# Optimization experiments

Hardware: AMD Instinct MI355X
Metric: run time of the kernel (lower is better)

The kernel has to match this reference:

```python
import jax, jax.numpy as jnp
import numpy as np

EPS = 1e-12  # F.normalize default eps

def _l2norm(x):
    n = jnp.linalg.norm(x, axis=-1, keepdims=True)
    return x / jnp.maximum(n, EPS)

def setup_inputs() -> dict:
    key = jax.random.key(0)
    k1, k2, k3 = jax.random.split(key, 3)
    Q, N, d_key, d_val = 4096, 65536, 128, 128
    return {
        "q": jax.random.normal(k1, (Q, d_key), dtype=jnp.float32),
        "keys": jax.random.normal(k2, (N, d_key), dtype=jnp.float32),
        "vals": jax.random.normal(k3, (N, d_val), dtype=jnp.float32),
        "topk": 8,
    }

def reference(q, keys, vals, topk):
    # cosine similarity: normalize both sides then dense matmul
    kn = _l2norm(keys)            # [N, d_key]
    qn = _l2norm(q)               # [Q, d_key]
    sims = qn @ kn.T              # [Q, N]
    kk = min(topk, sims.shape[1])
    topv, topi = jax.lax.top_k(sims, kk)          # [Q, k], [Q, k]
    weights = jax.nn.softmax(topv, axis=-1)        # [Q, k]
    gathered = vals[topi]                          # [Q, k, d_val] gather
    pred = jnp.einsum('qb,qbd->qd', weights, gathered)
    conf = jnp.clip(jnp.mean(topv, axis=-1), 0.0, 1.0)
    return pred, conf
```

## Files before the change

kernel.cpp:

```cpp
#include <hip/hip_runtime.h>
#include <stdint.h>


typedef unsigned int u32;
typedef unsigned long long u64;
typedef unsigned short u16;
typedef __attribute__((ext_vector_type(4))) float f32x4;
typedef __attribute__((ext_vector_type(2))) float f32x2;
typedef __attribute__((ext_vector_type(4))) int i32x4;
typedef __attribute__((ext_vector_type(8))) short s16x8;

#define D 128
#define KTILE 64
#define QW 64
#define QB 256
#define CMAX 64
#define MARGIN 0.05f
#define TBYTES (KTILE * 256)

__device__ __forceinline__ u16 f2bf(float f) {
    u32 b = __float_as_uint(f);
    b += 0x7FFFu + ((b >> 16) & 1u);
    return (u16)(b >> 16);
}
__device__ __forceinline__ u32 ford(float f) {
    u32 b = __float_as_uint(f);
    return (b & 0x80000000u) ? ~b : (b | 0x80000000u);
}
__device__ __forceinline__ float ford_inv(u32 ob) {
    u32 b = (ob & 0x80000000u) ? (ob ^ 0x80000000u) : ~ob;
    return __uint_as_float(b);
}

__global__ __launch_bounds__(256) void k_norm_keys(
        const float* __restrict__ keys, const float* __restrict__ q,
        u16* __restrict__ kn, float* __restrict__ invk, u16* __restrict__ qbf,
        int N, int Q) {
    int row = blockIdx.x * 4 + (threadIdx.x >> 6);
    int lane = threadIdx.x & 63;
    if (row >= N) return;
    if (row < Q) {
        f32x2 qv = *(const f32x2*)(q + (size_t)row * D + lane * 2);
        u32 qp = (u32)f2bf(qv.x) | ((u32)f2bf(qv.y) << 16);
        *(u32*)(qbf + (size_t)row * D + lane * 2) = qp;
    }
    const float* kr = keys + (size_t)row * D;
    f32x2 v = *(const f32x2*)(kr + lane * 2);
    float ss = v.x * v.x + v.y * v.y;
    #pragma unroll
    for (int o = 1; o < 64; o <<= 1) ss += __shfl_xor(ss, o);
    float inv = 1.0f / fmaxf(sqrtf(ss), 1e-12f);
    if (lane == 0) invk[row] = inv;
    u32 packed = (u32)f2bf(v.x * inv) | ((u32)f2bf(v.y * inv) << 16);
    *(u32*)(kn + (size_t)row * D + lane * 2) = packed;
}

__device__ __forceinline__ void load_afr_bf(const u16* qbf, int qrow_base,
                                            int lrow, int lhi, s16x8 afr[4]) {
    const u16* qrow = qbf + (size_t)(qrow_base + lrow) * D + lhi * 8;
    #pragma unroll
    for (int s = 0; s < 4; ++s) afr[s] = *(const s16x8*)(qrow + s * 32);
}

__device__ __forceinline__ void decode_bid(int bid, int nqb, int PPART,
                                           int& p, int& qb) {
    if ((PPART & 7) == 0) {
        int xcd = bid & 7, seq = bid >> 3;
        qb = seq % nqb;
        p  = (seq / nqb) * 8 + xcd;
    } else {
        p = bid / nqb; qb = bid % nqb;
    }
}


__global__ __launch_bounds__(256, 2) void k_pass1(
        const u16* __restrict__ kn, const u16* __restrict__ qbf,
        float* __restrict__ shi, float* __restrict__ ssec,
        int Q, int N, int PPART) {
    __shared__ __align__(16) char lds[TBYTES];
    const int tid = threadIdx.x;
    const int wave = tid >> 6, lane = tid & 63;
    const int lrow = lane & 15, lhi = lane >> 4;
    const int nqb = Q / QB;
    int p, qb;
    decode_bid(blockIdx.x, nqb, PPART, p, qb);
    const int part = N / PPART;
    const int key0 = p * part;
    const int qbase = qb * QB + wave * QW;

    s16x8 afr[4][4];
    #pragma unroll
    for (int qs = 0; qs < 4; ++qs) load_afr_bf(qbf, qbase + qs * 16, lrow, lhi, afr[qs]);

    float hi[4][4], sec[4][4];
    #pragma unroll
    for (int qs = 0; qs < 4; ++qs)
        #pragma unroll
        for (int r = 0; r < 4; ++r) { hi[qs][r] = -3.0e38f; sec[qs][r] = -3.0e38f; }

    int roff[4];
    #pragma unroll
    for (int s = 0; s < 4; ++s)
        roff[s] = lrow * 256 + ((((s << 2) + lhi) ^ lrow) << 4);

    const int srow = tid >> 2;
    const int sg0  = (tid & 3) << 2;
    const int sx   = srow & 15;
    int woff[4];
    #pragma unroll
    for (int i = 0; i < 4; ++i) woff[i] = srow * 256 + (((sg0 + i) ^ sx) << 4);
    const char* gsrc = (const char*)kn + ((size_t)(key0 + srow)) * 256 + sg0 * 16;

    const int iters = part / KTILE;
    i32x4 v[4];
    #pragma unroll
    for (int i = 0; i < 4; ++i) v[i] = *(const i32x4*)(gsrc + i * 16);
    const char* gnext = gsrc + TBYTES;

    const f32x4 kZero = {0.f, 0.f, 0.f, 0.f};

    for (int kb = 0; kb < iters; ++kb) {
        __syncthreads();
        #pragma unroll
        for (int i = 0; i < 4; ++i) *(i32x4*)(lds + woff[i]) = v[i];
        __syncthreads();
        if (kb + 1 < iters) {
            #pragma unroll
            for (int i = 0; i < 4; ++i) v[i] = *(const i32x4*)(gnext + i * 16);
            gnext += TBYTES;
        }
        __builtin_amdgcn_s_setprio(1);
        #pragma unroll
        for (int ktp = 0; ktp < 2; ++ktp) {
            const u32 tagA = (u32)((kb << 2) + (ktp << 1));
            const u32 tagB = tagA + 1u;
            s16x8 bfrA[4], bfrB[4];
            #pragma unroll
            for (int s = 0; s < 4; ++s) {
                bfrA[s] = *(const s16x8*)(lds + roff[s] + (ktp << 1) * 4096);
                bfrB[s] = *(const s16x8*)(lds + roff[s] + ((ktp << 1) + 1) * 4096);
            }
            #pragma unroll
            for (int qs = 0; qs < 4; ++qs) {
                f32x4 accA = __builtin_amdgcn_mfma_f32_16x16x32_bf16(
                                 afr[qs][0], bfrA[0], kZero, 0, 0, 0);
                f32x4 accB = __builtin_amdgcn_mfma_f32_16x16x32_bf16(
                                 afr[qs][0], bfrB[0], kZero, 0, 0, 0);
                #pragma unroll
                for (int s = 1; s < 4; ++s) {
                    accA = __builtin_amdgcn_mfma_f32_16x16x32_bf16(afr[qs][s], bfrA[s], accA, 0, 0, 0);
                    accB = __builtin_amdgcn_mfma_f32_16x16x32_bf16(afr[qs][s], bfrB[s], accB, 0, 0, 0);
                }
                #pragma unroll
                for (int r = 0; r < 4; ++r) {
                    float fa = __uint_as_float(
                        (__float_as_uint(accA[r]) & 0xFFFFFF00u) | tagA);
                    float fb = __uint_as_float(
                        (__float_as_uint(accB[r]) & 0xFFFFFF00u) | tagB);
                    float h0 = hi[qs][r];
                    sec[qs][r] = fmaxf(__builtin_amdgcn_fmed3f(h0, fa, fb), sec[qs][r]);
                    hi[qs][r]  = fmaxf(fmaxf(h0, fa), fb);
                }
            }
        }
        __builtin_amdgcn_s_setprio(0);
    }
    #pragma unroll
    for (int qs = 0; qs < 4; ++qs)
        #pragma unroll
        for (int r = 0; r < 4; ++r) {
            int qq = qbase + qs * 16 + (lhi << 2) + r;
            shi [((size_t)p * Q + qq) * 16 + lrow] = hi[qs][r];
            ssec[((size_t)p * Q + qq) * 16 + lrow] = sec[qs][r];
        }
}

__global__ __launch_bounds__(256) void k_finalize(
        const float* __restrict__ q, const float* __restrict__ keys,
        const float* __restrict__ vals, const float* __restrict__ invk,
        const float* __restrict__ shi, const float* __restrict__ ssec,
        float* __restrict__ pred, float* __restrict__ conf,
        int Q, int N, int PPART) {
    const int w = threadIdx.x >> 6;
    const int qq = blockIdx.x * 4 + w;
    const int lane = threadIdx.x & 63;
    __shared__ float qs[4][D];
    __shared__ u32 cand[4][CMAX];
    __shared__ u32 ccnt[4];
    if (lane == 0) ccnt[w] = 0u;

    const float* qrow = q + (size_t)qq * D;
    f32x2 qv = *(const f32x2*)(qrow + lane * 2);
    qs[w][lane * 2] = qv.x; qs[w][lane * 2 + 1] = qv.y;
    float ss = qv.x * qv.x + qv.y * qv.y;
    #pragma unroll
    for (int o = 1; o < 64; o <<= 1) ss += __shfl_xor(ss, o);
    const float invq = 1.0f / fmaxf(sqrtf(ss), 1e-12f);

    const int nv = PPART >> 2;
    float v[16], hv[16], sc[16];
    #pragma unroll
    for (int i = 0; i < 16; ++i) {
        if (i < nv) {
            size_t base = ((size_t)(i * 4 + (lane >> 4)) * Q + qq) * 16 + (lane & 15);
            hv[i] = v[i] = shi[base];
            sc[i] = ssec[base];
        } else { hv[i] = v[i] = sc[i] = -3.0e38f; }
    }
    float h = -3.0e38f;
    #pragma unroll
    for (int round = 0; round < 8; ++round) {
        h = v[0];
        #pragma unroll
        for (int i = 1; i < 16; ++i) h = fmaxf(h, v[i]);
        #pragma unroll
        for (int o = 1; o < 64; o <<= 1) h = fmaxf(h, __shfl_xor(h, o));
        #pragma unroll
        for (int i = 0; i < 16; ++i) if (v[i] == h) v[i] = -3.0e38f;
    }
    const float T = h - MARGIN;
    const int part = N / PPART;
    #pragma unroll
    for (int i = 0; i < 16; ++i) {
        if (i >= nv) break;
        const int sidx = i * 64 + lane;
        const int p = sidx >> 4, j = sidx & 15;
        if (hv[i] >= T) {
            u32 key = (u32)(p * part + (int)((__float_as_uint(hv[i]) & 255u) << 4) + j);
            u32 pos = atomicAdd(&ccnt[w], 1u);
            if (pos < CMAX) cand[w][pos] = key;
        }
        if (sc[i] >= T) {
            u32 key = (u32)(p * part + (int)((__float_as_uint(sc[i]) & 255u) << 4) + j);
            u32 pos = atomicAdd(&ccnt[w], 1u);
            if (pos < CMAX) cand[w][pos] = key;
        }
    }
    __syncthreads();

    const u32 n = min(ccnt[w], (u32)CMAX);
    const int c0 = lane >> 1;
    const int half = lane & 1;
    const bool valid0 = (u32)c0 < n;
    const bool valid1 = (u32)(c0 + 32) < n;
    const u32 key0 = valid0 ? cand[w][c0] : 0u;
    const u32 key1 = valid1 ? cand[w][c0 + 32] : 0u;

    const float* qsp = &qs[w][half * 64];
    float dot0 = 0.f, dot1 = 0.f;
    {
        const float* kr0 = keys + (size_t)key0 * D + half * 64;
        const float* kr1 = keys + (size_t)key1 * D + half * 64;
        #pragma unroll
        for (int j = 0; j < 64; j += 4) {
            f32x4 a = *(const f32x4*)(kr0 + j);
            f32x4 b = *(const f32x4*)(kr1 + j);
            dot0 += a.x * qsp[j] + a.y * qsp[j + 1] + a.z * qsp[j + 2] + a.w * qsp[j + 3];
            dot1 += b.x * qsp[j] + b.y * qsp[j + 1] + b.z * qsp[j + 2] + b.w * qsp[j + 3];
        }
    }
    dot0 += __shfl_xor(dot0, 1);
    dot1 += __shfl_xor(dot1, 1);
    const float ex0 = dot0 * invk[key0] * invq;
    const float ex1 = dot1 * invk[key1] * invq;
    u64 pkA = valid0 ? (((u64)ford(ex0) << 32) | (u32)(~key0)) : 0ull;
    u64 pkB = valid1 ? (((u64)ford(ex1) << 32) | (u32)(~key1)) : 0ull;

    float accA = 0.f, accB = 0.f, wsum = 0.f, vsum = 0.f, vmax = 0.f;
    #pragma unroll
    for (int r = 0; r < 8; ++r) {
        u64 mx = pkA > pkB ? pkA : pkB;
        u64 hh = mx;
        #pragma unroll
        for (int o = 1; o < 64; o <<= 1) {
            u64 tt = __shfl_xor(hh, o);
            hh = tt > hh ? tt : hh;
        }
        const bool ok = (hh != 0ull);
        const float vv = ford_inv((u32)(hh >> 32));
        const u32 idx = ok ? ~((u32)hh) : 0u;
        if (r == 0) vmax = vv;
        const float wgt = ok ? expf(vv - vmax) : 0.f;
        wsum += wgt; vsum += ok ? vv : 0.f;
        const float* vr = vals + (size_t)idx * D;
        accA += wgt * vr[lane];
        accB += wgt * vr[lane + 64];
        if (pkA == hh) pkA = 0ull;
        if (pkB == hh) pkB = 0ull;
    }
    const float inv_ws = 1.0f / wsum;
    pred[(size_t)qq * D + lane] = accA * inv_ws;
    pred[(size_t)qq * D + lane + 64] = accB * inv_ws;
    if (lane == 0) conf[qq] = fminf(fmaxf(vsum * 0.125f, 0.f), 1.f);
}

extern "C" void kernel_launch(void* const* d_in, const int* in_sizes, int n_in,
                              void* d_out, int out_size, void* d_ws, size_t ws_size,
                              hipStream_t stream) {
    const float* q    = (const float*)d_in[0];
    const float* keys = (const float*)d_in[1];
    const float* vals = (const float*)d_in[2];
    const int Q = in_sizes[0] / D;
    const int N = in_sizes[1] / D;

    int PPART = 64;
    auto need = [&](int P) {
        return (size_t)N * D * 2 + (size_t)N * 4 + (size_t)Q * D * 2 +
               2 * ((size_t)Q * P * 16 * 4);
    };
    while (PPART > 16 && need(PPART) > ws_size) PPART >>= 1;

    char* ws = (char*)d_ws;
    size_t off = 0;
    u16*   kn   = (u16*)(ws + off);   off += (size_t)N * D * 2;
    float* invk = (float*)(ws + off); off += (size_t)N * 4;
    u16*   qbf  = (u16*)(ws + off);   off += (size_t)Q * D * 2;
    float* shi  = (float*)(ws + off); off += (size_t)Q * PPART * 16 * 4;
    float* ssec = (float*)(ws + off); off += (size_t)Q * PPART * 16 * 4;

    float* pred = (float*)d_out;
    float* conf = pred + (size_t)Q * D;

    k_norm_keys<<<(N + 3) / 4, 256, 0, stream>>>(keys, q, kn, invk, qbf, N, Q);
    k_pass1<<<(Q / QB) * PPART, 256, 0, stream>>>(kn, qbf, shi, ssec, Q, N, PPART);
    k_finalize<<<Q / 4, 256, 0, stream>>>(q, keys, vals, invk, shi, ssec,
                                          pred, conf, Q, N, PPART);
}
```

Measured before the change: 106.0 us.

## Merge paired key tiles before top-2 tracking, expand candidates to both keys

The similarity pass now takes the max of the two paired MFMA results (tiles A and B) before tagging and updating the running top-2. This roughly halves the per-element tag and compare work in the hot loop. In exchange, each surviving tag now stands for two possible keys, so the finalize kernel enqueues both keys per hit. CMAX rises from 64 to 96 and a third candidate slot per lane is added for exact rescoring, which adds more gathers and dot products in finalize.

```diff
diff --git a/kernel.cpp b/kernel.cpp
--- a/kernel.cpp
+++ b/kernel.cpp
@@ -14,7 +14,7 @@
 #define KTILE 64
 #define QW 64
 #define QB 256
-#define CMAX 64
+#define CMAX 96
 #define MARGIN 0.05f
 #define TBYTES (KTILE * 256)
 
@@ -133,8 +133,7 @@
         __builtin_amdgcn_s_setprio(1);
         #pragma unroll
         for (int ktp = 0; ktp < 2; ++ktp) {
-            const u32 tagA = (u32)((kb << 2) + (ktp << 1));
-            const u32 tagB = tagA + 1u;
+            const u32 tagP = (u32)((kb << 1) + ktp);
             s16x8 bfrA[4], bfrB[4];
             #pragma unroll
             for (int s = 0; s < 4; ++s) {
@@ -154,13 +153,12 @@
                 }
                 #pragma unroll
                 for (int r = 0; r < 4; ++r) {
-                    float fa = __uint_as_float(
-                        (__float_as_uint(accA[r]) & 0xFFFFFF00u) | tagA);
-                    float fb = __uint_as_float(
-                        (__float_as_uint(accB[r]) & 0xFFFFFF00u) | tagB);
+                    float fm = fmaxf(accA[r], accB[r]);
+                    float tf = __uint_as_float(
+                        (__float_as_uint(fm) & 0xFFFFFF00u) | tagP);
                     float h0 = hi[qs][r];
-                    sec[qs][r] = fmaxf(__builtin_amdgcn_fmed3f(h0, fa, fb), sec[qs][r]);
-                    hi[qs][r]  = fmaxf(fmaxf(h0, fa), fb);
+                    sec[qs][r] = __builtin_amdgcn_fmed3f(tf, sec[qs][r], h0);
+                    hi[qs][r]  = fmaxf(h0, tf);
                 }
             }
         }
@@ -227,14 +225,16 @@
         const int sidx = i * 64 + lane;
         const int p = sidx >> 4, j = sidx & 15;
         if (hv[i] >= T) {
-            u32 key = (u32)(p * part + (int)((__float_as_uint(hv[i]) & 255u) << 4) + j);
-            u32 pos = atomicAdd(&ccnt[w], 1u);
-            if (pos < CMAX) cand[w][pos] = key;
+            u32 k0 = (u32)(p * part + (int)((__float_as_uint(hv[i]) & 255u) << 5) + j);
+            u32 pos = atomicAdd(&ccnt[w], 2u);
+            if (pos < CMAX) cand[w][pos] = k0;
+            if (pos + 1 < CMAX) cand[w][pos + 1] = k0 + 16u;
         }
         if (sc[i] >= T) {
-            u32 key = (u32)(p * part + (int)((__float_as_uint(sc[i]) & 255u) << 4) + j);
-            u32 pos = atomicAdd(&ccnt[w], 1u);
-            if (pos < CMAX) cand[w][pos] = key;
+            u32 k0 = (u32)(p * part + (int)((__float_as_uint(sc[i]) & 255u) << 5) + j);
+            u32 pos = atomicAdd(&ccnt[w], 2u);
+            if (pos < CMAX) cand[w][pos] = k0;
+            if (pos + 1 < CMAX) cand[w][pos + 1] = k0 + 16u;
         }
     }
     __syncthreads();
@@ -244,33 +244,42 @@
     const int half = lane & 1;
     const bool valid0 = (u32)c0 < n;
     const bool valid1 = (u32)(c0 + 32) < n;
+    const bool valid2 = (u32)(c0 + 64) < n;
     const u32 key0 = valid0 ? cand[w][c0] : 0u;
     const u32 key1 = valid1 ? cand[w][c0 + 32] : 0u;
+    const u32 key2 = valid2 ? cand[w][c0 + 64] : 0u;
 
     const float* qsp = &qs[w][half * 64];
-    float dot0 = 0.f, dot1 = 0.f;
+    float dot0 = 0.f, dot1 = 0.f, dot2 = 0.f;
     {
         const float* kr0 = keys + (size_t)key0 * D + half * 64;
         const float* kr1 = keys + (size_t)key1 * D + half * 64;
+        const float* kr2 = keys + (size_t)key2 * D + half * 64;
         #pragma unroll
         for (int j = 0; j < 64; j += 4) {
             f32x4 a = *(const f32x4*)(kr0 + j);
             f32x4 b = *(const f32x4*)(kr1 + j);
+            f32x4 c = *(const f32x4*)(kr2 + j);
             dot0 += a.x * qsp[j] + a.y * qsp[j + 1] + a.z * qsp[j + 2] + a.w * qsp[j + 3];
             dot1 += b.x * qsp[j] + b.y * qsp[j + 1] + b.z * qsp[j + 2] + b.w * qsp[j + 3];
+            dot2 += c.x * qsp[j] + c.y * qsp[j + 1] + c.z * qsp[j + 2] + c.w * qsp[j + 3];
         }
     }
     dot0 += __shfl_xor(dot0, 1);
     dot1 += __shfl_xor(dot1, 1);
+    dot2 += __shfl_xor(dot2, 1);
     const float ex0 = dot0 * invk[key0] * invq;
     const float ex1 = dot1 * invk[key1] * invq;
+    const float ex2 = dot2 * invk[key2] * invq;
     u64 pkA = valid0 ? (((u64)ford(ex0) << 32) | (u32)(~key0)) : 0ull;
     u64 pkB = valid1 ? (((u64)ford(ex1) << 32) | (u32)(~key1)) : 0ull;
+    u64 pkC = valid2 ? (((u64)ford(ex2) << 32) | (u32)(~key2)) : 0ull;
 
     float accA = 0.f, accB = 0.f, wsum = 0.f, vsum = 0.f, vmax = 0.f;
     #pragma unroll
     for (int r = 0; r < 8; ++r) {
         u64 mx = pkA > pkB ? pkA : pkB;
+        mx = pkC > mx ? pkC : mx;
         u64 hh = mx;
         #pragma unroll
         for (int o = 1; o < 64; o <<= 1) {
@@ -288,6 +297,7 @@
         accB += wgt * vr[lane + 64];
         if (pkA == hh) pkA = 0ull;
         if (pkB == hh) pkB = 0ull;
+        if (pkC == hh) pkC = 0ull;
     }
     const float inv_ws = 1.0f / wsum;
     pred[(size_t)qq * D + lane] = accA * inv_ws;
```

Measured after the change: 118.2 us. +11.5%, slower.
